# Optimization experiments

Measured on AMD Instinct MI355X. Metric: run time of the kernel, lower is better.

The kernel has to match this reference:

```python
import jax, jax.numpy as jnp
import numpy as np

B, C, D, H, W = 4, 1, 192, 192, 192
SMALL = 4            # int(192 * bias_scale=0.025)
BIAS_STD = 0.7
MAX_SIGMA = 3.0
TRUNCATE = 4.0
K = 2 * int(TRUNCATE * MAX_SIGMA) + 1   # fixed truncated kernel size = 25
N_LABELS = 32
TABLE = 128          # static remap-table size (>= max source label, >= max dest)


def setup_inputs() -> dict:
    key = jax.random.key(0)
    k1, k2, k3, k4, k5 = jax.random.split(key, 5)
    return {
        "x": jax.random.normal(k1, (B, C, D, H, W), jnp.float32),
        "small_bias": jax.random.normal(k2, (B, 1, SMALL, SMALL, SMALL), jnp.float32),
        "sigma01": jax.random.uniform(k3, (B, 3), jnp.float32),
        "labels": jax.random.randint(k4, (B, 1, D, H, W), 0, N_LABELS, jnp.int32),
        "source_values": jnp.arange(N_LABELS, dtype=jnp.int64),
        "dest_values": jax.random.randint(k5, (N_LABELS,), 0, 100, jnp.int64),
    }


def _lin_weights(n_in, n_out):
    """Dense 1D linear-interp matrix [n_out, n_in], align_corners=True."""
    pos = jnp.linspace(0.0, n_in - 1.0, n_out)
    i0 = jnp.clip(jnp.floor(pos).astype(jnp.int32), 0, n_in - 2)
    f = pos - i0.astype(pos.dtype)
    r = jnp.arange(n_out)
    Wm = jnp.zeros((n_out, n_in), jnp.float32)
    Wm = Wm.at[r, i0].add(1.0 - f).at[r, i0 + 1].add(f)
    return Wm


def _bias_field(small_bias):
    # trilinear align_corners upsample [B,1,s,s,s] -> [B,1,D,H,W], separable
    b = small_bias * BIAS_STD
    b = jnp.einsum('bcxyz,dx->bcdyz', b, _lin_weights(SMALL, D))
    b = jnp.einsum('bcdyz,hy->bcdhz', b, _lin_weights(SMALL, H))
    b = jnp.einsum('bcdhz,wz->bcdhw', b, _lin_weights(SMALL, W))
    return b


def _gauss_kernels(sigma):
    """sigma [3] -> normalized kernels [3, K]; identity (delta) where sigma<0.01."""
    ar = jnp.arange(K, dtype=jnp.float32) - K // 2
    s = jnp.maximum(sigma, 1e-3)[:, None]
    g = jnp.exp(-0.5 * (ar[None, :] ** 2) / (s ** 2))
    g = g / g.sum(-1, keepdims=True)
    delta = jnp.zeros((K,), jnp.float32).at[K // 2].set(1.0)
    return jnp.where(sigma[:, None] >= 0.01, g, delta[None, :])


def _blur_axis(x, k, axis):
    # x [C,D,H,W]; depthwise 1D conv along `axis` with replicate (edge) padding
    p = K // 2
    xm = jnp.moveaxis(x, axis, -1)
    shp = xm.shape
    xm = xm.reshape(-1, 1, shp[-1])
    xm = jnp.pad(xm, ((0, 0), (0, 0), (p, p)), mode='edge')
    out = jax.lax.conv_general_dilated(xm, k.reshape(1, 1, K), (1,), 'VALID')
    return jnp.moveaxis(out.reshape(shp), -1, axis)


def _blur_sample(x, kernels):
    # x [C,D,H,W], kernels [3,K]; separable blur over D,H,W
    for i, ax in enumerate((1, 2, 3)):
        x = _blur_axis(x, kernels[i], ax)
    return x


def reference(x, small_bias, sigma01, labels, source_values, dest_values):
    # 1) bias-field corruption: x * exp(upsampled random field)
    img = x * jnp.exp(_bias_field(small_bias))
    # 2) dynamic per-sample Gaussian blur, sigma in [0, MAX_SIGMA]
    kernels = jax.vmap(_gauss_kernels)(sigma01 * MAX_SIGMA)   # [B,3,K]
    img = jax.vmap(_blur_sample)(img, kernels)
    # 3) label remap via lookup table gather
    mapping = jnp.zeros((TABLE,), jnp.int32).at[source_values].set(
        dest_values.astype(jnp.int32))
    labels_out = mapping[labels]
    return img, labels_out
```

## Files before the change

kernel.cpp:

```cpp
#include <hip/hip_runtime.h>
#include <hip/hip_fp16.h>
#include <cstdint>
#include <cstddef>

#define Bc 4
#define Dd 192
#define Hh 192
#define Ww 192
#define KK 25
#define RR 12
#define VOL (Bc*Dd*Hh*Ww)
#define SP 216
#define SPU (SP/2)
#define SH 98
#define RIN 120

typedef unsigned short u16;
typedef unsigned int   u32;

__global__ void setup_tables_kernel(const float* __restrict__ sigma01,
                                    const int* __restrict__ src,
                                    const int* __restrict__ dst,
                                    float* __restrict__ kern,
                                    u32* __restrict__ kern2,
                                    int* __restrict__ mapping) {
    int t = threadIdx.x;
    if (t < 128) mapping[t] = 0;
    __syncthreads();
    if (t < 32) {
        int s = src[t];
        if (s >= 0 && s < 128) mapping[s] = dst[t];
    }
    if (t < Bc * 3) {
        float sig = sigma01[t] * 3.0f;
        float s = fmaxf(sig, 1e-3f);
        float g[KK];
        float sum = 0.0f;
        #pragma unroll
        for (int i = 0; i < KK; i++) {
            float a = (float)(i - RR);
            float v = expf(-0.5f * a * a / (s * s));
            g[i] = v; sum += v;
        }
        float inv = 1.0f / sum;
        #pragma unroll
        for (int i = 0; i < KK; i++) {
            float v = g[i] * inv;
            if (sig < 0.01f) v = (i == RR) ? 1.0f : 0.0f;
            kern[t * KK + i] = v;
            u16 hb = __builtin_bit_cast(u16, __float2half(v));
            kern2[t * KK + i] = (u32)hb | ((u32)hb << 16);
        }
    }
}

__global__ __launch_bounds__(512) void pass_wh_remap_kernel(
    const float* __restrict__ x, u16* __restrict__ outB,
    const float* __restrict__ kern, const u32* __restrict__ kern2,
    const float* __restrict__ sb,
    const int4* __restrict__ labels, float4* __restrict__ lab_out,
    const int* __restrict__ mapping) {
    __shared__ u16 P[RIN * SP];
    __shared__ u32 ch[RIN][2];
    const int tid = threadIdx.x;
    const int hx = blockIdx.x;
    const int d  = blockIdx.y;
    const int b  = blockIdx.z;

    if (tid < RIN * 4) {
        int r = tid >> 2, k = tid & 3;
        int hrow = min(max(96 * hx - RR + r, 0), Hh - 1);
        float pos_d = d * (3.0f / 191.0f);
        int   id0   = min((int)pos_d, 2);
        float fd    = pos_d - (float)id0;
        float pos_h = hrow * (3.0f / 191.0f);
        float w0h = fmaxf(0.f, 1.f - fabsf(pos_h));
        float w1h = fmaxf(0.f, 1.f - fabsf(pos_h - 1.f));
        float w2h = fmaxf(0.f, 1.f - fabsf(pos_h - 2.f));
        float w3h = fmaxf(0.f, 1.f - fabsf(pos_h - 3.f));
        const float* sbA = sb + b * 64 + id0 * 16;
        float sj0 = (1.f - fd) * sbA[k]      + fd * sbA[16 + k];
        float sj1 = (1.f - fd) * sbA[4 + k]  + fd * sbA[20 + k];
        float sj2 = (1.f - fd) * sbA[8 + k]  + fd * sbA[24 + k];
        float sj3 = (1.f - fd) * sbA[12 + k] + fd * sbA[28 + k];
        float cv = (w0h * sj0 + w1h * sj1 + w2h * sj2 + w3h * sj3) * 0.7f;
        u16 hb = __builtin_bit_cast(u16, __float2half(cv));
        atomicAnd(&ch[r][k >> 1], ~(0xFFFFu << ((k & 1) * 16)));
        (void)hb;
    }
    __syncthreads();
    if (tid < RIN) {
        int r = tid;
        int hrow = min(max(96 * hx - RR + r, 0), Hh - 1);
        float pos_d = d * (3.0f / 191.0f);
        int   id0   = min((int)pos_d, 2);
        float fd    = pos_d - (float)id0;
        float pos_h = hrow * (3.0f / 191.0f);
        float w0h = fmaxf(0.f, 1.f - fabsf(pos_h));
        float w1h = fmaxf(0.f, 1.f - fabsf(pos_h - 1.f));
        float w2h = fmaxf(0.f, 1.f - fabsf(pos_h - 2.f));
        float w3h = fmaxf(0.f, 1.f - fabsf(pos_h - 3.f));
        const float* sbA = sb + b * 64 + id0 * 16;
        float c[4];
        #pragma unroll
        for (int k = 0; k < 4; k++) {
            float sj0 = (1.f - fd) * sbA[k]      + fd * sbA[16 + k];
            float sj1 = (1.f - fd) * sbA[4 + k]  + fd * sbA[20 + k];
            float sj2 = (1.f - fd) * sbA[8 + k]  + fd * sbA[24 + k];
            float sj3 = (1.f - fd) * sbA[12 + k] + fd * sbA[28 + k];
            c[k] = (w0h * sj0 + w1h * sj1 + w2h * sj2 + w3h * sj3) * 0.7f;
        }
        ch[r][0] = (u32)__builtin_bit_cast(u16, __float2half(c[0])) |
                   ((u32)__builtin_bit_cast(u16, __float2half(c[1])) << 16);
        ch[r][1] = (u32)__builtin_bit_cast(u16, __float2half(c[2])) |
                   ((u32)__builtin_bit_cast(u16, __float2half(c[3])) << 16);
    }
    __syncthreads();

    const size_t pbase = ((size_t)b * Dd + d) * (size_t)(Hh * Ww);
    #pragma unroll
    for (int it = 0; it < 12; it++) {
        int i4 = it * 512 + tid;
        if (i4 < RIN * 48) {
            int r = i4 / 48, w4 = i4 % 48;
            int w = 4 * w4;
            int hrow = min(max(96 * hx - RR + r, 0), Hh - 1);
            float4 v = *(const float4*)(x + pbase + (size_t)hrow * Ww + w);
            float2 cv01 = __half22float2(__builtin_bit_cast(__half2, ch[r][0]));
            float2 cv23 = __half22float2(__builtin_bit_cast(__half2, ch[r][1]));
            float rs[4];
            #pragma unroll
            for (int j = 0; j < 4; j++) {
                float pw = (w + j) * (3.0f / 191.0f);
                float b0 = fmaxf(0.f, 1.f - fabsf(pw));
                float b1 = fmaxf(0.f, 1.f - fabsf(pw - 1.f));
                float b2 = fmaxf(0.f, 1.f - fabsf(pw - 2.f));
                float b3 = fmaxf(0.f, 1.f - fabsf(pw - 3.f));
                float bias = b0 * cv01.x + b1 * cv01.y + b2 * cv23.x + b3 * cv23.y;
                float val = (j == 0 ? v.x : j == 1 ? v.y : j == 2 ? v.z : v.w);
                rs[j] = val * __expf(bias);
            }
            u32 p0 = (u32)__builtin_bit_cast(u16, __float2half(rs[0])) |
                     ((u32)__builtin_bit_cast(u16, __float2half(rs[1])) << 16);
            u32 p1 = (u32)__builtin_bit_cast(u16, __float2half(rs[2])) |
                     ((u32)__builtin_bit_cast(u16, __float2half(rs[3])) << 16);
            u32* dstp = (u32*)&P[r * SP + RR + w];
            dstp[0] = p0; dstp[1] = p1;
            if (w4 == 0) {
                u16 hv = __builtin_bit_cast(u16, __float2half(rs[0]));
                u32 hh = (u32)hv | ((u32)hv << 16);
                u32* hp = (u32*)&P[r * SP];
                #pragma unroll
                for (int m = 0; m < 6; m++) hp[m] = hh;
            } else if (w4 == 47) {
                u16 hv = __builtin_bit_cast(u16, __float2half(rs[3]));
                u32 hh = (u32)hv | ((u32)hv << 16);
                u32* hp = (u32*)&P[r * SP + RR + Ww];
                #pragma unroll
                for (int m = 0; m < 6; m++) hp[m] = hh;
            }
        }
    }
    __syncthreads();

    {
        float kw[KK];
        const float* kp = kern + (b * 3 + 2) * KK;
        #pragma unroll
        for (int t = 0; t < KK; t++) kw[t] = kp[t];
        const int wv = tid >> 6, ln = tid & 63;
        const int r4 = ln >> 5, c = ln & 31;
        #pragma unroll
        for (int it = 0; it < 8; it++) {
            const int lr = it * 2 + r4;
            if (lr < 15) {
                const int row = wv * 15 + lr;
                const u32* rp = (const u32*)&P[row * SP] + 3 * c;
                u32 wraw[15];
                #pragma unroll
                for (int i = 0; i < 15; i++) wraw[i] = rp[i];
                float win[30];
                #pragma unroll
                for (int i = 0; i < 15; i++) {
                    float2 f = __half22float2(__builtin_bit_cast(__half2, wraw[i]));
                    win[2 * i] = f.x; win[2 * i + 1] = f.y;
                }
                float acc[6];
                #pragma unroll
                for (int j = 0; j < 6; j++) acc[j] = 0.0f;
                #pragma unroll
                for (int t = 0; t < KK; t++) {
                    float kv = kw[t];
                    #pragma unroll
                    for (int j = 0; j < 6; j++) acc[j] += kv * win[j + t];
                }
                u32* wp = (u32*)&P[row * SP + RR + 6 * c];
                #pragma unroll
                for (int m = 0; m < 3; m++) {
                    wp[m] = (u32)__builtin_bit_cast(u16, __float2half(acc[2 * m])) |
                            ((u32)__builtin_bit_cast(u16, __float2half(acc[2 * m + 1])) << 16);
                }
            }
        }
    }
    __syncthreads();

    {
        u32 k2[KK];
        const u32* kp = kern2 + (b * 3 + 1) * KK;
        #pragma unroll
        for (int t = 0; t < KK; t++) k2[t] = kp[t];
        u32* outp = (u32*)(outB + pbase);
        #pragma unroll
        for (int it = 0; it < 2; it++) {
            int item = it * 512 + tid;
            if (item < 768) {
                int col = item % 96;
                int g = item / 96;
                u32 win[36];
                #pragma unroll
                for (int i = 0; i < 36; i++)
                    win[i] = *((const u32*)&P[(g * 12 + i) * SP] + 6 + col);
                __half2 acc[12];
                #pragma unroll
                for (int j = 0; j < 12; j++) acc[j] = __float2half2_rn(0.0f);
                #pragma unroll
                for (int t = 0; t < KK; t++) {
                    __half2 kv = __builtin_bit_cast(__half2, k2[t]);
                    #pragma unroll
                    for (int j = 0; j < 12; j++)
                        acc[j] = __hfma2(kv, __builtin_bit_cast(__half2, win[j + t]), acc[j]);
                }
                #pragma unroll
                for (int j = 0; j < 12; j++)
                    outp[(96 * hx + g * 12 + j) * 96 + col] =
                        __builtin_bit_cast(u32, acc[j]);
            }
        }
    }

    {
        const int bid = ((b * Dd) + d) * 2 + hx;
        int base = bid * 4608 + tid;
        #pragma unroll
        for (int it = 0; it < 9; it++) {
            int i = base + it * 512;
            int4 l = labels[i];
            float4 o;
            o.x = (float)mapping[min(max(l.x, 0), 127)];
            o.y = (float)mapping[min(max(l.y, 0), 127)];
            o.z = (float)mapping[min(max(l.z, 0), 127)];
            o.w = (float)mapping[min(max(l.w, 0), 127)];
            lab_out[i] = o;
        }
    }
}

__global__ __launch_bounds__(192) void pass_d_kernel(
    const u16* __restrict__ in, float* __restrict__ img,
    const u32* __restrict__ kern2) {
    __shared__ __attribute__((aligned(16))) u16 T[88 * SH];
    const int tid = threadIdx.x;
    const int w0 = blockIdx.x * 96;
    const int d0 = blockIdx.y * 64;
    const int z = blockIdx.z;
    const int h = z % Hh, b = z / Hh;
    u32 k2[KK];
    const u32* kp = kern2 + b * 3 * KK;
    #pragma unroll
    for (int t = 0; t < KK; t++) k2[t] = kp[t];
    #pragma unroll
    for (int k = 0; k < 6; k++) {
        int idx = k * 192 + tid;
        if (idx < 1056) {
            int r = idx / 12, sg = idx % 12;
            int dd = min(max(d0 + r - RR, 0), Dd - 1);
            uint4 v = *(const uint4*)(in + (((size_t)b * Dd + dd) * Hh + h) * (size_t)Ww + w0 + sg * 8);
            u32* p = (u32*)&T[r * SH + sg * 8];
            p[0] = v.x; p[1] = v.y; p[2] = v.z; p[3] = v.w;
        }
    }
    __syncthreads();
    const int p = tid % 48;
    const int g0 = tid / 48;
    #pragma unroll
    for (int cc = 0; cc < 2; cc++) {
        const int g = g0 + cc * 4;
        const int ob = g * 8;
        u32 win[32];
        #pragma unroll
        for (int i = 0; i < 32; i++) win[i] = *(const u32*)&T[(ob + i) * SH + 2 * p];
        __half2 acc[8];
        #pragma unroll
        for (int j = 0; j < 8; j++) acc[j] = __float2half2_rn(0.0f);
        #pragma unroll
        for (int t = 0; t < KK; t++) {
            __half2 kv = __builtin_bit_cast(__half2, k2[t]);
            #pragma unroll
            for (int j = 0; j < 8; j++)
                acc[j] = __hfma2(kv, __builtin_bit_cast(__half2, win[j + t]), acc[j]);
        }
        #pragma unroll
        for (int j = 0; j < 8; j++) {
            float2 f = __half22float2(acc[j]);
            *(float2*)(img + (((size_t)b * Dd + (d0 + ob + j)) * Hh + h) * (size_t)Ww + w0 + 2 * p) = f;
        }
    }
}

extern "C" void kernel_launch(void* const* d_in, const int* in_sizes, int n_in,
                              void* d_out, int out_size, void* d_ws, size_t ws_size,
                              hipStream_t stream) {
    const float* x          = (const float*)d_in[0];
    const float* small_bias = (const float*)d_in[1];
    const float* sigma01    = (const float*)d_in[2];
    const int*   labels     = (const int*)d_in[3];
    const int*   src        = (const int*)d_in[4];
    const int*   dst        = (const int*)d_in[5];

    float* out     = (float*)d_out;
    float* img     = out;
    float* lab_out = out + (size_t)VOL;

    float* kern    = (float*)d_ws;
    u32*   kern2   = (u32*)((float*)d_ws + 384);
    int*   mapping = (int*)((float*)d_ws + 768);
    u16*   Bb      = (u16*)((char*)d_ws + 8192);

    setup_tables_kernel<<<1, 128, 0, stream>>>(sigma01, src, dst, kern, kern2, mapping);

    pass_wh_remap_kernel<<<dim3(2, Dd, Bc), 512, 0, stream>>>(
        x, Bb, kern, kern2, small_bias,
        (const int4*)labels, (float4*)lab_out, mapping);
    pass_d_kernel<<<dim3(Ww / 96, Dd / 64, Bc * Hh), 192, 0, stream>>>(Bb, img, kern2);
}
```

Measured before the change: 152.1 us.

## Convert W-axis blur to packed half2 FMA and simplify bias-field interpolation

The W-axis blur now runs on packed half2 FMAs instead of scalar fp32. It splits the kernel into even and odd taps over the aligned words and byte-shifted words, and each thread produces 12 outputs instead of 6. Bias coefficients are stored as fp32 with plain bilinear interpolation and a select-based lerp along W, and a dead atomicAnd init pass and its barrier are removed. Kernel taps are read directly from global memory instead of being preloaded into registers. This lowers ALU work and register pressure, at the cost of fp16 accumulation precision in the W pass.

```diff
diff --git a/kernel.cpp b/kernel.cpp
--- a/kernel.cpp
+++ b/kernel.cpp
@@ -56,39 +56,17 @@
 
 __global__ __launch_bounds__(512) void pass_wh_remap_kernel(
     const float* __restrict__ x, u16* __restrict__ outB,
-    const float* __restrict__ kern, const u32* __restrict__ kern2,
+    const u32* __restrict__ kern2,
     const float* __restrict__ sb,
     const int4* __restrict__ labels, float4* __restrict__ lab_out,
     const int* __restrict__ mapping) {
     __shared__ u16 P[RIN * SP];
-    __shared__ u32 ch[RIN][2];
+    __shared__ __attribute__((aligned(16))) float ch[RIN][4];
     const int tid = threadIdx.x;
     const int hx = blockIdx.x;
     const int d  = blockIdx.y;
     const int b  = blockIdx.z;
 
-    if (tid < RIN * 4) {
-        int r = tid >> 2, k = tid & 3;
-        int hrow = min(max(96 * hx - RR + r, 0), Hh - 1);
-        float pos_d = d * (3.0f / 191.0f);
-        int   id0   = min((int)pos_d, 2);
-        float fd    = pos_d - (float)id0;
-        float pos_h = hrow * (3.0f / 191.0f);
-        float w0h = fmaxf(0.f, 1.f - fabsf(pos_h));
-        float w1h = fmaxf(0.f, 1.f - fabsf(pos_h - 1.f));
-        float w2h = fmaxf(0.f, 1.f - fabsf(pos_h - 2.f));
-        float w3h = fmaxf(0.f, 1.f - fabsf(pos_h - 3.f));
-        const float* sbA = sb + b * 64 + id0 * 16;
-        float sj0 = (1.f - fd) * sbA[k]      + fd * sbA[16 + k];
-        float sj1 = (1.f - fd) * sbA[4 + k]  + fd * sbA[20 + k];
-        float sj2 = (1.f - fd) * sbA[8 + k]  + fd * sbA[24 + k];
-        float sj3 = (1.f - fd) * sbA[12 + k] + fd * sbA[28 + k];
-        float cv = (w0h * sj0 + w1h * sj1 + w2h * sj2 + w3h * sj3) * 0.7f;
-        u16 hb = __builtin_bit_cast(u16, __float2half(cv));
-        atomicAnd(&ch[r][k >> 1], ~(0xFFFFu << ((k & 1) * 16)));
-        (void)hb;
-    }
-    __syncthreads();
     if (tid < RIN) {
         int r = tid;
         int hrow = min(max(96 * hx - RR + r, 0), Hh - 1);
@@ -96,24 +74,17 @@
         int   id0   = min((int)pos_d, 2);
         float fd    = pos_d - (float)id0;
         float pos_h = hrow * (3.0f / 191.0f);
-        float w0h = fmaxf(0.f, 1.f - fabsf(pos_h));
-        float w1h = fmaxf(0.f, 1.f - fabsf(pos_h - 1.f));
-        float w2h = fmaxf(0.f, 1.f - fabsf(pos_h - 2.f));
-        float w3h = fmaxf(0.f, 1.f - fabsf(pos_h - 3.f));
-        const float* sbA = sb + b * 64 + id0 * 16;
-        float c[4];
+        int   ih0   = min((int)pos_h, 2);
+        float fh    = pos_h - (float)ih0;
+        const float* sbA = sb + b * 64 + id0 * 16 + ih0 * 4;
         #pragma unroll
         for (int k = 0; k < 4; k++) {
-            float sj0 = (1.f - fd) * sbA[k]      + fd * sbA[16 + k];
-            float sj1 = (1.f - fd) * sbA[4 + k]  + fd * sbA[20 + k];
-            float sj2 = (1.f - fd) * sbA[8 + k]  + fd * sbA[24 + k];
-            float sj3 = (1.f - fd) * sbA[12 + k] + fd * sbA[28 + k];
-            c[k] = (w0h * sj0 + w1h * sj1 + w2h * sj2 + w3h * sj3) * 0.7f;
-        }
-        ch[r][0] = (u32)__builtin_bit_cast(u16, __float2half(c[0])) |
-                   ((u32)__builtin_bit_cast(u16, __float2half(c[1])) << 16);
-        ch[r][1] = (u32)__builtin_bit_cast(u16, __float2half(c[2])) |
-                   ((u32)__builtin_bit_cast(u16, __float2half(c[3])) << 16);
+            float v00 = sbA[k],      v01 = sbA[4 + k];
+            float v10 = sbA[16 + k], v11 = sbA[20 + k];
+            float vd0 = (1.f - fd) * v00 + fd * v10;
+            float vd1 = (1.f - fd) * v01 + fd * v11;
+            ch[r][k] = ((1.f - fh) * vd0 + fh * vd1) * 0.7f;
+        }
     }
     __syncthreads();
 
@@ -126,17 +97,17 @@
             int w = 4 * w4;
             int hrow = min(max(96 * hx - RR + r, 0), Hh - 1);
             float4 v = *(const float4*)(x + pbase + (size_t)hrow * Ww + w);
-            float2 cv01 = __half22float2(__builtin_bit_cast(__half2, ch[r][0]));
-            float2 cv23 = __half22float2(__builtin_bit_cast(__half2, ch[r][1]));
+            float4 cv = *(const float4*)&ch[r][0];
             float rs[4];
             #pragma unroll
             for (int j = 0; j < 4; j++) {
                 float pw = (w + j) * (3.0f / 191.0f);
-                float b0 = fmaxf(0.f, 1.f - fabsf(pw));
-                float b1 = fmaxf(0.f, 1.f - fabsf(pw - 1.f));
-                float b2 = fmaxf(0.f, 1.f - fabsf(pw - 2.f));
-                float b3 = fmaxf(0.f, 1.f - fabsf(pw - 3.f));
-                float bias = b0 * cv01.x + b1 * cv01.y + b2 * cv23.x + b3 * cv23.y;
+                bool s1 = pw >= 1.0f, s2 = pw >= 2.0f;
+                float clo = s2 ? cv.z : (s1 ? cv.y : cv.x);
+                float chi = s2 ? cv.w : (s1 ? cv.z : cv.y);
+                float fb  = s2 ? 2.0f : (s1 ? 1.0f : 0.0f);
+                float fw  = pw - fb;
+                float bias = clo + fw * (chi - clo);
                 float val = (j == 0 ? v.x : j == 1 ? v.y : j == 2 ? v.z : v.w);
                 rs[j] = val * __expf(bias);
             }
@@ -164,52 +135,51 @@
     __syncthreads();
 
     {
-        float kw[KK];
-        const float* kp = kern + (b * 3 + 2) * KK;
-        #pragma unroll
-        for (int t = 0; t < KK; t++) kw[t] = kp[t];
+        const u32* kw2 = kern2 + (b * 3 + 2) * KK;
         const int wv = tid >> 6, ln = tid & 63;
-        const int r4 = ln >> 5, c = ln & 31;
-        #pragma unroll
-        for (int it = 0; it < 8; it++) {
-            const int lr = it * 2 + r4;
+        const int r4 = ln >> 4;
+        const int c  = ln & 15;
+        #pragma unroll
+        for (int it = 0; it < 4; it++) {
+            const int lr = it * 4 + r4;
             if (lr < 15) {
                 const int row = wv * 15 + lr;
-                const u32* rp = (const u32*)&P[row * SP] + 3 * c;
-                u32 wraw[15];
-                #pragma unroll
-                for (int i = 0; i < 15; i++) wraw[i] = rp[i];
-                float win[30];
-                #pragma unroll
-                for (int i = 0; i < 15; i++) {
-                    float2 f = __half22float2(__builtin_bit_cast(__half2, wraw[i]));
-                    win[2 * i] = f.x; win[2 * i + 1] = f.y;
+                const u32* rp = (const u32*)P + row * SPU + 6 * c;
+                u32 E[18];
+                #pragma unroll
+                for (int j = 0; j < 18; j++) E[j] = rp[j];
+                u32 O[17];
+                #pragma unroll
+                for (int j = 0; j < 17; j++)
+                    O[j] = (E[j] >> 16) | (E[j + 1] << 16);
+                __half2 acc[6];
+                #pragma unroll
+                for (int m = 0; m < 6; m++) acc[m] = __float2half2_rn(0.0f);
+                #pragma unroll
+                for (int s = 0; s < 13; s++) {
+                    __half2 kv = __builtin_bit_cast(__half2, kw2[2 * s]);
+                    #pragma unroll
+                    for (int m = 0; m < 6; m++)
+                        acc[m] = __hfma2(kv, __builtin_bit_cast(__half2, E[m + s]), acc[m]);
                 }
-                float acc[6];
-                #pragma unroll
-                for (int j = 0; j < 6; j++) acc[j] = 0.0f;
-                #pragma unroll
-                for (int t = 0; t < KK; t++) {
-                    float kv = kw[t];
+                #pragma unroll
+                for (int s = 0; s < 12; s++) {
+                    __half2 kv = __builtin_bit_cast(__half2, kw2[2 * s + 1]);
                     #pragma unroll
-                    for (int j = 0; j < 6; j++) acc[j] += kv * win[j + t];
+                    for (int m = 0; m < 6; m++)
+                        acc[m] = __hfma2(kv, __builtin_bit_cast(__half2, O[m + s]), acc[m]);
                 }
-                u32* wp = (u32*)&P[row * SP + RR + 6 * c];
-                #pragma unroll
-                for (int m = 0; m < 3; m++) {
-                    wp[m] = (u32)__builtin_bit_cast(u16, __float2half(acc[2 * m])) |
-                            ((u32)__builtin_bit_cast(u16, __float2half(acc[2 * m + 1])) << 16);
-                }
+                u32* wp = (u32*)P + row * SPU + 6 + 6 * c;
+                #pragma unroll
+                for (int m = 0; m < 6; m++)
+                    wp[m] = __builtin_bit_cast(u32, acc[m]);
             }
         }
     }
     __syncthreads();
 
     {
-        u32 k2[KK];
-        const u32* kp = kern2 + (b * 3 + 1) * KK;
-        #pragma unroll
-        for (int t = 0; t < KK; t++) k2[t] = kp[t];
+        const u32* kh2 = kern2 + (b * 3 + 1) * KK;
         u32* outp = (u32*)(outB + pbase);
         #pragma unroll
         for (int it = 0; it < 2; it++) {
@@ -220,13 +190,13 @@
                 u32 win[36];
                 #pragma unroll
                 for (int i = 0; i < 36; i++)
-                    win[i] = *((const u32*)&P[(g * 12 + i) * SP] + 6 + col);
+                    win[i] = *((const u32*)P + (g * 12 + i) * SPU + 6 + col);
                 __half2 acc[12];
                 #pragma unroll
                 for (int j = 0; j < 12; j++) acc[j] = __float2half2_rn(0.0f);
                 #pragma unroll
                 for (int t = 0; t < KK; t++) {
-                    __half2 kv = __builtin_bit_cast(__half2, k2[t]);
+                    __half2 kv = __builtin_bit_cast(__half2, kh2[t]);
                     #pragma unroll
                     for (int j = 0; j < 12; j++)
                         acc[j] = __hfma2(kv, __builtin_bit_cast(__half2, win[j + t]), acc[j]);
@@ -265,10 +235,7 @@
     const int d0 = blockIdx.y * 64;
     const int z = blockIdx.z;
     const int h = z % Hh, b = z / Hh;
-    u32 k2[KK];
     const u32* kp = kern2 + b * 3 * KK;
-    #pragma unroll
-    for (int t = 0; t < KK; t++) k2[t] = kp[t];
     #pragma unroll
     for (int k = 0; k < 6; k++) {
         int idx = k * 192 + tid;
@@ -295,7 +262,7 @@
         for (int j = 0; j < 8; j++) acc[j] = __float2half2_rn(0.0f);
         #pragma unroll
         for (int t = 0; t < KK; t++) {
-            __half2 kv = __builtin_bit_cast(__half2, k2[t]);
+            __half2 kv = __builtin_bit_cast(__half2, kp[t]);
             #pragma unroll
             for (int j = 0; j < 8; j++)
                 acc[j] = __hfma2(kv, __builtin_bit_cast(__half2, win[j + t]), acc[j]);
@@ -330,7 +297,7 @@
     setup_tables_kernel<<<1, 128, 0, stream>>>(sigma01, src, dst, kern, kern2, mapping);
 
     pass_wh_remap_kernel<<<dim3(2, Dd, Bc), 512, 0, stream>>>(
-        x, Bb, kern, kern2, small_bias,
+        x, Bb, kern2, small_bias,
         (const int4*)labels, (float4*)lab_out, mapping);
     pass_d_kernel<<<dim3(Ww / 96, Dd / 64, Bc * Hh), 192, 0, stream>>>(Bb, img, kern2);
 }
```

Result: faster. 141.2 us (-7.1%).
